# Optimization experiments

Measured on AMD Instinct MI355X. Metric: run time of the kernel, lower is better.

The kernel has to match this reference:

```python
import jax, jax.numpy as jnp
import numpy as np

B, T, NE, NZ, H = 64, 1024, 256, 64, 256  # batch, timesteps, n_e, n_z, encoder_hidden
SW_HID = 128  # switch MLP hidden width (hardcoded in source)


def setup_inputs() -> dict:
    key = jax.random.key(0)
    ks = jax.random.split(key, 16)
    s = 0.05
    p = lambda k, shape: (jax.random.normal(k, shape, dtype=jnp.float32) * s)
    return {
        "e_seq": jax.random.normal(ks[0], (B, T, NE), dtype=jnp.float32),
        "eps": jax.random.normal(ks[1], (B, T, NZ), dtype=jnp.float32),  # randn_like noise, precomputed
        # GRU forward direction (torch layout: weight_ih [3H, NE] order r,z,n)
        "w_ih_f": p(ks[2], (3 * H, NE)), "w_hh_f": p(ks[3], (3 * H, H)),
        "b_ih_f": jnp.zeros((3 * H,), jnp.float32), "b_hh_f": jnp.zeros((3 * H,), jnp.float32),
        # GRU backward direction
        "w_ih_b": p(ks[4], (3 * H, NE)), "w_hh_b": p(ks[5], (3 * H, H)),
        "b_ih_b": jnp.zeros((3 * H,), jnp.float32), "b_hh_b": jnp.zeros((3 * H,), jnp.float32),
        # mu / logvar heads over [B,T,2H]
        "mu_w": p(ks[6], (NZ, 2 * H)), "mu_b": jnp.zeros((NZ,), jnp.float32),
        "lv_w": p(ks[7], (NZ, 2 * H)), "lv_b": jnp.zeros((NZ,), jnp.float32),
        # switching unit: Linear(NE + 2H + NZ, 128) -> ReLU -> Linear(128,1) -> Sigmoid
        "sw_w1": p(ks[8], (SW_HID, NE + 2 * H + NZ)), "sw_b1": jnp.zeros((SW_HID,), jnp.float32),
        "sw_w2": p(ks[9], (1, SW_HID)), "sw_b2": jnp.zeros((1,), jnp.float32),
    }


def _gru_dir(x, w_ih, w_hh, b_ih, b_hh, reverse):
    # x: [B,T,NE]; torch GRU cell: r,z = sigmoid; n = tanh(x_n + r*(W_hn h + b_hn)); h' = (1-z)*n + z*h
    xp = jnp.einsum('btn,gn->btg', x, w_ih) + b_ih  # [B,T,3H] input projections, once
    xp = jnp.swapaxes(xp, 0, 1)  # [T,B,3H]
    h0 = jnp.zeros((x.shape[0], w_hh.shape[1]), x.dtype)

    def step(h, xpt):
        hp = h @ w_hh.T + b_hh
        xr, xz, xn = jnp.split(xpt, 3, axis=-1)
        hr, hz, hn = jnp.split(hp, 3, axis=-1)
        r = jax.nn.sigmoid(xr + hr)
        z = jax.nn.sigmoid(xz + hz)
        n = jnp.tanh(xn + r * hn)
        h_new = (1.0 - z) * n + z * h
        return h_new, h_new

    _, hs = jax.lax.scan(step, h0, xp, reverse=reverse)  # outputs time-aligned even when reversed
    return jnp.swapaxes(hs, 0, 1)  # [B,T,H]


def _forward(e_seq, eps, w_ih_f, w_hh_f, b_ih_f, b_hh_f, w_ih_b, w_hh_b, b_ih_b, b_hh_b,
             mu_w, mu_b, lv_w, lv_b, sw_w1, sw_b1, sw_w2, sw_b2):
    h_f = _gru_dir(e_seq, w_ih_f, w_hh_f, b_ih_f, b_hh_f, reverse=False)
    h_b = _gru_dir(e_seq, w_ih_b, w_hh_b, b_ih_b, b_hh_b, reverse=True)
    h_seq = jnp.concatenate([h_f, h_b], axis=-1)  # [B,T,2H]

    mu = h_seq @ mu_w.T + mu_b    # [B,T,NZ]
    lv = h_seq @ lv_w.T + lv_b    # [B,T,NZ]

    n_e = e_seq.shape[-1]
    h2 = h_seq.shape[-1]
    # split switch first-layer weight by input segments [e_t | h_t | z_prev]
    w1_e = sw_w1[:, :n_e]
    w1_h = sw_w1[:, n_e:n_e + h2]
    w1_z = sw_w1[:, n_e + h2:]
    # precompute e/h contributions for all t; only z_prev contribution is sequential
    pre = jnp.einsum('btn,kn->btk', e_seq, w1_e) + jnp.einsum('bth,kh->btk', h_seq, w1_h) + sw_b1  # [B,T,128]

    z_tilde = mu + jnp.exp(0.5 * lv) * eps                    # reparameterized sample [B,T,NZ]
    kl = (-0.5 * (1.0 + lv - mu * mu - jnp.exp(lv))).sum(-1)  # [B,T]

    def step(z_prev, inputs):
        pre_t, zt_t = inputs  # [B,128], [B,NZ]
        hid = jax.nn.relu(pre_t + z_prev @ w1_z.T)
        beta = jax.nn.sigmoid(hid @ sw_w2.T + sw_b2)[..., 0]  # [B]
        z_t = beta[:, None] * zt_t + (1.0 - beta[:, None]) * z_prev
        return z_t, (z_t, beta)

    z0 = jnp.zeros((e_seq.shape[0], mu.shape[-1]), e_seq.dtype)
    _, (zs, betas) = jax.lax.scan(step, z0, (jnp.swapaxes(pre, 0, 1), jnp.swapaxes(z_tilde, 0, 1)))
    z_seq = jnp.swapaxes(zs, 0, 1)     # [B,T,NZ]
    beta_seq = jnp.swapaxes(betas, 0, 1)  # [B,T]
    kl_loss = kl.mean()
    return z_seq, kl_loss, beta_seq


def reference(e_seq, eps, w_ih_f, w_hh_f, b_ih_f, b_hh_f, w_ih_b, w_hh_b, b_ih_b, b_hh_b,
              mu_w, mu_b, lv_w, lv_b, sw_w1, sw_b1, sw_w2, sw_b2):
    return _forward(e_seq, eps, w_ih_f, w_hh_f, b_ih_f, b_hh_f, w_ih_b, w_hh_b, b_ih_b, b_hh_b,
                    mu_w, mu_b, lv_w, lv_b, sw_w1, sw_b1, sw_w2, sw_b2)
```

## Files before the change

### kernel.cpp

```cpp
#include <hip/hip_runtime.h>
#include <cstdint>

typedef _Float16 half_t;
typedef _Float16 half2_t __attribute__((ext_vector_type(2)));
typedef _Float16 h8_t __attribute__((ext_vector_type(8)));
typedef float f4_t __attribute__((ext_vector_type(4)));
typedef unsigned int uint32;
typedef uint32 uv16 __attribute__((ext_vector_type(16)));

static constexpr int B_ = 64, T_ = 1024;

#define DEV __device__ __forceinline__

DEV float fdot2f(half2_t a, half2_t b, float c) {
#if __has_builtin(__builtin_amdgcn_fdot2)
  return __builtin_amdgcn_fdot2(a, b, c, false);
#else
  return fmaf((float)a.x, (float)b.x, fmaf((float)a.y, (float)b.y, c));
#endif
}

DEV float fast_rcp(float x) { return __builtin_amdgcn_rcpf(x); }
DEV float sigmf(float x) { return fast_rcp(1.f + __expf(-x)); }
DEV float tanhf_(float x) { return 1.f - 2.f * fast_rcp(1.f + __expf(2.f * x)); }
DEV uint32 pack2(float a, float b) {
  half2_t h; h.x = (half_t)a; h.y = (half_t)b;
  return __builtin_bit_cast(uint32, h);
}
DEV half2_t bch2(uint32 u) { return __builtin_bit_cast(half2_t, u); }

DEV void gload_lds16(const void* g, void* l) {
  __builtin_amdgcn_global_load_lds(
      (const __attribute__((address_space(1))) uint32*)g,
      (__attribute__((address_space(3))) uint32*)l, 16, 0, 0);
}

#define WSEL(va, vb, j) bch2(((j) < 16) ? (va)[(j) & 15] : (vb)[((j) - 16) & 15])

__global__ __launch_bounds__(256) void pack_w(
    const float* __restrict__ w_ih_f, const float* __restrict__ w_ih_b,
    const float* __restrict__ mu_w, const float* __restrict__ lv_w,
    const float* __restrict__ sw_w1,
    const float* __restrict__ w_hh_f, const float* __restrict__ w_hh_b,
    const float* __restrict__ b_ih_f, const float* __restrict__ b_ih_b,
    const float* __restrict__ b_hh_f, const float* __restrict__ b_hh_b,
    const float* __restrict__ mu_b, const float* __restrict__ lv_b,
    const float* __restrict__ sw_b1,
    uint32* __restrict__ wihf, uint32* __restrict__ wihb,
    uint32* __restrict__ wchf, uint32* __restrict__ wchb, uint32* __restrict__ wce2,
    uint32* __restrict__ whh, uint32* __restrict__ w1z,
    float* __restrict__ biasc, float* __restrict__ biasf, float* __restrict__ biasb) {
  int id = blockIdx.x * 256 + threadIdx.x;
  if (id < 98304) { wihf[id] = pack2(w_ih_f[2*id], w_ih_f[2*id+1]); return; }
  id -= 98304;
  if (id < 98304) { wihb[id] = pack2(w_ih_b[2*id], w_ih_b[2*id+1]); return; }
  id -= 98304;
  if (id < 32768) {
    int n = id >> 7, c0 = (id & 127) * 2;
    const float* p = (n < 64)  ? mu_w + n * 512 + c0
                   : (n < 128) ? lv_w + (n - 64) * 512 + c0
                               : sw_w1 + (n - 128) * 832 + 256 + c0;
    wchf[id] = pack2(p[0], p[1]); return;
  }
  id -= 32768;
  if (id < 32768) {
    int n = id >> 7, c0 = (id & 127) * 2;
    const float* p = (n < 64)  ? mu_w + n * 512 + 256 + c0
                   : (n < 128) ? lv_w + (n - 64) * 512 + 256 + c0
                               : sw_w1 + (n - 128) * 832 + 512 + c0;
    wchb[id] = pack2(p[0], p[1]); return;
  }
  id -= 32768;
  if (id < 16384) {
    int n = id >> 7, c0 = (id & 127) * 2;
    wce2[id] = pack2(sw_w1[n * 832 + c0], sw_w1[n * 832 + c0 + 1]); return;
  }
  id -= 16384;
  if (id < 196608) {
    int dd = id / 98304, q = id % 98304;
    int j = q >> 9, t2 = q & 511;
    int rr = t2 >> 2, pp = t2 & 3;
    int gi = j >> 5, ck = j & 31;
    int g = gi >> 1, i = gi & 1;
    int row = 256 * g + 2 * rr + i;
    int k0 = pp * 64 + 2 * ck;
    const float* w = dd ? w_hh_b : w_hh_f;
    whh[id] = pack2(w[row * 256 + k0], w[row * 256 + k0 + 1]);
    return;
  }
  id -= 196608;
  if (id < 4096) {
    int j = id >> 6, kk = id & 63;
    int row = (j < 32) ? kk : kk + 64;
    int jj = j & 31;
    w1z[id] = pack2(sw_w1[row * 832 + 768 + 2 * jj], sw_w1[row * 832 + 768 + 2 * jj + 1]);
    return;
  }
  id -= 4096;
  if (id < 256) {
    biasc[id] = (id < 64) ? mu_b[id] : (id < 128) ? lv_b[id - 64] : sw_b1[id - 128];
    return;
  }
  id -= 256;
  if (id < 768) { biasf[id] = b_ih_f[id] + (id < 512 ? b_hh_f[id] : 0.f); return; }
  id -= 768;
  if (id < 768) { biasb[id] = b_ih_b[id] + (id < 512 ? b_hh_b[id] : 0.f); return; }
}

template <int AF32, int ACC>
__global__ __launch_bounds__(256) void gemm_t(
    const void* __restrict__ Ap, int lda,
    const half_t* __restrict__ Bw,
    const float* __restrict__ bias,
    half_t* __restrict__ C, int ldc, int K) {
  __shared__ __align__(16) half_t smem[16384];
  half_t* As = smem;
  half_t* Bs = smem + 8192;
  const int tid = threadIdx.x;
  const int lane = tid & 63, w = tid >> 6;
  const int n0 = blockIdx.x * 128, m0 = blockIdx.y * 128;
  const int r8 = lane >> 3, c8 = lane & 7;
  f4_t acc[4][4];
  f4_t zero = {0.f, 0.f, 0.f, 0.f};
#pragma unroll
  for (int i = 0; i < 4; ++i)
#pragma unroll
    for (int j = 0; j < 4; ++j) acc[i][j] = zero;
  const int wm = (w >> 1) * 64, wn = (w & 1) * 64;
  for (int ks = 0; ks < K; ks += 64) {
    if constexpr (AF32) {
      const float* Af = (const float*)Ap;
#pragma unroll
      for (int it = 0; it < 4; ++it) {
        int c = it * 256 + tid;
        int row = c >> 3, coff = (c & 7) * 8;
        const float* ap = Af + (size_t)(m0 + row) * lda + ks + coff;
        float4 v0 = *(const float4*)ap;
        float4 v1 = *(const float4*)(ap + 4);
        uint4 u;
        u.x = pack2(v0.x, v0.y); u.y = pack2(v0.z, v0.w);
        u.z = pack2(v1.x, v1.y); u.w = pack2(v1.z, v1.w);
        *(uint4*)&As[(size_t)c * 8] = u;
      }
    } else {
      const half_t* Af = (const half_t*)Ap;
#pragma unroll
      for (int c = 0; c < 4; ++c) {
        int row = w * 32 + c * 8 + r8;
        gload_lds16(Af + (size_t)(m0 + row) * lda + ks + c8 * 8, As + (w * 4 + c) * 512);
      }
    }
#pragma unroll
    for (int c = 0; c < 4; ++c) {
      int row = w * 32 + c * 8 + r8;
      gload_lds16(Bw + (size_t)(n0 + row) * K + ks + c8 * 8, Bs + (w * 4 + c) * 512);
    }
    __syncthreads();
#pragma unroll
    for (int kk = 0; kk < 2; ++kk) {
      h8_t af[4], bf[4];
      const int ko = kk * 32 + (lane >> 4) * 8;
#pragma unroll
      for (int i = 0; i < 4; ++i) af[i] = *(const h8_t*)&As[(wm + i * 16 + (lane & 15)) * 64 + ko];
#pragma unroll
      for (int j = 0; j < 4; ++j) bf[j] = *(const h8_t*)&Bs[(wn + j * 16 + (lane & 15)) * 64 + ko];
#pragma unroll
      for (int i = 0; i < 4; ++i)
#pragma unroll
        for (int j = 0; j < 4; ++j)
          acc[i][j] = __builtin_amdgcn_mfma_f32_16x16x32_f16(af[i], bf[j], acc[i][j], 0, 0, 0);
    }
    __syncthreads();
  }
  const int cl4 = lane & 15, rl4 = lane >> 4;
#pragma unroll
  for (int j = 0; j < 4; ++j) {
    float bj = bias ? bias[n0 + wn + j * 16 + cl4] : 0.f;
#pragma unroll
    for (int i = 0; i < 4; ++i)
#pragma unroll
      for (int q = 0; q < 4; ++q) {
        int rl = wm + i * 16 + rl4 * 4 + q;
        int cc = wn + j * 16 + cl4;
        smem[rl * 128 + cc] = (half_t)(acc[i][j][q] + bj);
      }
  }
  __syncthreads();
#pragma unroll
  for (int it = 0; it < 8; ++it) {
    int idx = it * 256 + tid;
    int row = idx >> 4, colc = idx & 15;
    uint4 v = *(const uint4*)&smem[row * 128 + colc * 8];
    half_t* cp = C + (size_t)(m0 + row) * ldc + n0 + colc * 8;
    if constexpr (ACC) {
      uint4 o = *(const uint4*)cp;
      h8_t vv = __builtin_bit_cast(h8_t, v) + __builtin_bit_cast(h8_t, o);
      v = __builtin_bit_cast(uint4, vv);
    }
    *(uint4*)cp = v;
  }
}

__global__ __attribute__((amdgpu_flat_work_group_size(512, 512)))
__attribute__((amdgpu_waves_per_eu(2, 2))) void gru_rec(
    uint32* __restrict__ xp,
    const uint32* __restrict__ whh2,
    const float* __restrict__ bhh_f, const float* __restrict__ bhh_b) {
  const int wg = blockIdx.x;
  const int d = wg >> 6, b = wg & 63;
  const int tid = threadIdx.x;
  const int r = tid >> 2, p = tid & 3;
  __shared__ uint32 hb[2][144];
  if (tid < 144) { hb[0][tid] = 0; hb[1][tid] = 0; }
  uv16 w0a, w0b, w1a, w1b, w2a, w2b, w3a, w3b, w4a, w4b, w5a, w5b;
  {
    const uint32* wp = whh2 + (size_t)d * 98304 + tid;
#define LD16(vec, base)                                   \
  _Pragma("unroll") for (int e = 0; e < 16; ++e) vec[e] = \
      wp[(size_t)((base) + e) * 512];
    LD16(w0a, 0);   LD16(w0b, 16);  LD16(w1a, 32);  LD16(w1b, 48);
    LD16(w2a, 64);  LD16(w2b, 80);  LD16(w3a, 96);  LD16(w3b, 112);
    LD16(w4a, 128); LD16(w4b, 144); LD16(w5a, 160); LD16(w5b, 176);
#undef LD16
    asm volatile("" : "+v"(w0a), "+v"(w0b), "+v"(w1a), "+v"(w1b), "+v"(w2a), "+v"(w2b));
    asm volatile("" : "+v"(w3a), "+v"(w3b), "+v"(w4a), "+v"(w4b), "+v"(w5a), "+v"(w5b));
  }
  const float* bhh = d ? bhh_b : bhh_f;
  const float bhn0 = bhh[512 + 2 * r], bhn1 = bhh[512 + 2 * r + 1];
  uint32* xpu = xp + ((size_t)d * B_ + b) * T_ * 384;
  float h0 = 0.f, h1 = 0.f;
  const int dt = d ? -1 : 1;
  int t = d ? (T_ - 1) : 0;
  uint32 xr_n = 0, xz_n = 0, xn_n = 0;
  if (p == 0) {
    const uint32* rowp = xpu + (size_t)t * 384;
    xr_n = rowp[r]; xz_n = rowp[128 + r]; xn_n = rowp[256 + r];
  }
  const int rdbase = p * 36;
  const int wslice = (r >> 5) * 36 + (r & 31);
  __syncthreads();
  for (int step = 0; step < T_; ++step) {
    const int cur = step & 1;
    const uint32 xr = xr_n, xz = xz_n, xn = xn_n;
    const int tn = (step < T_ - 1) ? (t + dt) : t;
    if (p == 0) {
      const uint32* rowp = xpu + (size_t)tn * 384;
      xr_n = rowp[r]; xz_n = rowp[128 + r]; xn_n = rowp[256 + r];
    }
    float a00 = 0, a10 = 0, a01 = 0, a11 = 0, a02 = 0, a12 = 0;
    const uint32* hc = &hb[cur][rdbase];
#pragma unroll
    for (int c = 0; c < 4; ++c) {
      uint4 u0 = *(const uint4*)(hc + c * 8);
      uint4 u1 = *(const uint4*)(hc + c * 8 + 4);
      uint32 hv[8] = {u0.x, u0.y, u0.z, u0.w, u1.x, u1.y, u1.z, u1.w};
#pragma unroll
      for (int e = 0; e < 8; ++e) {
        const int j = c * 8 + e;
        half2_t hh = bch2(hv[e]);
        a00 = fdot2f(WSEL(w0a, w0b, j), hh, a00);
        a10 = fdot2f(WSEL(w1a, w1b, j), hh, a10);
        a01 = fdot2f(WSEL(w2a, w2b, j), hh, a01);
        a11 = fdot2f(WSEL(w3a, w3b, j), hh, a11);
        a02 = fdot2f(WSEL(w4a, w4b, j), hh, a02);
        a12 = fdot2f(WSEL(w5a, w5b, j), hh, a12);
      }
    }
    a00 += __shfl_xor(a00, 1); a00 += __shfl_xor(a00, 2);
    a10 += __shfl_xor(a10, 1); a10 += __shfl_xor(a10, 2);
    a01 += __shfl_xor(a01, 1); a01 += __shfl_xor(a01, 2);
    a11 += __shfl_xor(a11, 1); a11 += __shfl_xor(a11, 2);
    a02 += __shfl_xor(a02, 1); a02 += __shfl_xor(a02, 2);
    a12 += __shfl_xor(a12, 1); a12 += __shfl_xor(a12, 2);
    if (p == 0) {
      half2_t xrv = bch2(xr), xzv = bch2(xz), xnv = bch2(xn);
      float r0 = sigmf((float)xrv.x + a00);
      float z0 = sigmf((float)xzv.x + a01);
      float n0 = tanhf_((float)xnv.x + r0 * (a02 + bhn0));
      h0 = (1.f - z0) * n0 + z0 * h0;
      float r1 = sigmf((float)xrv.y + a10);
      float z1 = sigmf((float)xzv.y + a11);
      float n1 = tanhf_((float)xnv.y + r1 * (a12 + bhn1));
      h1 = (1.f - z1) * n1 + z1 * h1;
      uint32 ph = pack2(h0, h1);
      hb[cur ^ 1][wslice] = ph;
      xpu[(size_t)t * 384 + r] = ph;
    }
    __syncthreads();
    t = tn;
  }
}

__global__ __launch_bounds__(256) void zkl(const half_t* __restrict__ hp,
                                           const float* __restrict__ eps,
                                           float* __restrict__ ztil,
                                           float* __restrict__ klp) {
  const int blk = blockIdx.x, tid = threadIdx.x;
  const size_t bt = (size_t)blk * 4 + (tid >> 6);
  const int j = tid & 63;
  float mu = (float)hp[bt * 768 + j];
  float lv = (float)hp[bt * 768 + 64 + j];
  float ev = eps[bt * 64 + j];
  ztil[bt * 64 + j] = mu + __expf(0.5f * lv) * ev;
  float term = 1.f + lv - mu * mu - __expf(lv);
#pragma unroll
  for (int s = 1; s < 64; s <<= 1) term += __shfl_xor(term, s);
  __shared__ float red[4];
  if ((tid & 63) == 0) red[tid >> 6] = term;
  __syncthreads();
  if (tid == 0) klp[blk] = red[0] + red[1] + red[2] + red[3];
}

__global__ __launch_bounds__(256) void klred(const float* __restrict__ klp,
                                             float* __restrict__ out) {
  const int tid = threadIdx.x;
  float s = 0.f;
  for (int i = tid; i < 16384; i += 256) s += klp[i];
#pragma unroll
  for (int st = 1; st < 64; st <<= 1) s += __shfl_xor(s, st);
  __shared__ float red[4];
  if ((tid & 63) == 0) red[tid >> 6] = s;
  __syncthreads();
  if (tid == 0) out[0] = (red[0] + red[1] + red[2] + red[3]) * (-0.5f / 65536.f);
}

__global__ __launch_bounds__(64) void z_scan(
    const half_t* __restrict__ hp,
    const float* __restrict__ zt_arr,
    const uint32* __restrict__ w1z,
    const float* __restrict__ sw_w2, const float* __restrict__ sw_b2,
    float* __restrict__ z_out, float* __restrict__ beta_out) {
  const int b = blockIdx.x;
  const int k = threadIdx.x;
  uv16 z0a, z0b, z1a, z1b;
  {
#define LDZ(vec, base)                                    \
  _Pragma("unroll") for (int e = 0; e < 16; ++e) vec[e] = \
      w1z[((base) + e) * 64 + k];
    LDZ(z0a, 0); LDZ(z0b, 16); LDZ(z1a, 32); LDZ(z1b, 48);
#undef LDZ
    asm volatile("" : "+v"(z0a), "+v"(z0b), "+v"(z1a), "+v"(z1b));
  }
  const float w2k0 = sw_w2[k], w2k1 = sw_w2[k + 64], b2 = sw_b2[0];
  __shared__ uint32 zbuf[2][32];
  if (k < 32) { zbuf[0][k] = 0; zbuf[1][k] = 0; }
  __syncthreads();
  float zf = 0.f;
  const size_t bt0 = (size_t)b * T_;
  float pre0n = (float)hp[bt0 * 768 + 128 + k];
  float pre1n = (float)hp[bt0 * 768 + 192 + k];
  float ztn = zt_arr[bt0 * 64 + k];
  for (int t = 0; t < T_; ++t) {
    const int cur = t & 1;
    const float pre0 = pre0n, pre1 = pre1n, zt = ztn;
    const int tn = (t < T_ - 1) ? t + 1 : t;
    pre0n = (float)hp[(bt0 + tn) * 768 + 128 + k];
    pre1n = (float)hp[(bt0 + tn) * 768 + 192 + k];
    ztn = zt_arr[(bt0 + tn) * 64 + k];
    float a0 = 0, a1 = 0, a2 = 0, a3 = 0;
#pragma unroll
    for (int q = 0; q < 8; ++q) {
      uint4 u = *(const uint4*)&zbuf[cur][q * 4];
      const int m = q * 4;
      a0 = fdot2f(WSEL(z0a, z0b, m),     bch2(u.x), a0);
      a1 = fdot2f(WSEL(z0a, z0b, m + 1), bch2(u.y), a1);
      a0 = fdot2f(WSEL(z0a, z0b, m + 2), bch2(u.z), a0);
      a1 = fdot2f(WSEL(z0a, z0b, m + 3), bch2(u.w), a1);
      a2 = fdot2f(WSEL(z1a, z1b, m),     bch2(u.x), a2);
      a3 = fdot2f(WSEL(z1a, z1b, m + 1), bch2(u.y), a3);
      a2 = fdot2f(WSEL(z1a, z1b, m + 2), bch2(u.z), a2);
      a3 = fdot2f(WSEL(z1a, z1b, m + 3), bch2(u.w), a3);
    }
    float hid0 = fmaxf(pre0 + a0 + a1, 0.f);
    float hid1 = fmaxf(pre1 + a2 + a3, 0.f);
    float v = fmaf(hid0, w2k0, hid1 * w2k1);
#pragma unroll
    for (int s = 1; s < 64; s <<= 1) v += __shfl_xor(v, s);
    const float beta = sigmf(v + b2);
    zf = beta * zt + (1.f - beta) * zf;
    z_out[(bt0 + t) * 64 + k] = zf;
    if (k == 0) beta_out[bt0 + t] = beta;
    float zo = __shfl_xor(zf, 1);
    if ((k & 1) == 0) zbuf[cur ^ 1][k >> 1] = pack2(zf, zo);
    asm volatile("s_waitcnt lgkmcnt(0)" ::: "memory");
  }
}

extern "C" void kernel_launch(void* const* d_in, const int* in_sizes, int n_in,
                              void* d_out, int out_size, void* d_ws, size_t ws_size,
                              hipStream_t stream) {
  (void)in_sizes; (void)n_in; (void)out_size;
  const float* e_seq  = (const float*)d_in[0];
  const float* eps    = (const float*)d_in[1];
  const float* w_ih_f = (const float*)d_in[2];
  const float* w_hh_f = (const float*)d_in[3];
  const float* b_ih_f = (const float*)d_in[4];
  const float* b_hh_f = (const float*)d_in[5];
  const float* w_ih_b = (const float*)d_in[6];
  const float* w_hh_b = (const float*)d_in[7];
  const float* b_ih_b = (const float*)d_in[8];
  const float* b_hh_b = (const float*)d_in[9];
  const float* mu_w   = (const float*)d_in[10];
  const float* mu_b   = (const float*)d_in[11];
  const float* lv_w   = (const float*)d_in[12];
  const float* lv_b   = (const float*)d_in[13];
  const float* sw_w1  = (const float*)d_in[14];
  const float* sw_b1  = (const float*)d_in[15];
  const float* sw_w2  = (const float*)d_in[16];
  const float* sw_b2  = (const float*)d_in[17];

  const size_t NEED = 201326592 + 1924096;
  if (ws_size < NEED) return;
  char* ws = (char*)d_ws;
  half_t* xpf = (half_t*)ws;
  half_t* xpb = (half_t*)(ws + 100663296);
  half_t* hp  = xpf + 512;
  float*  ztil = (float*)(ws + 100663296);
  float*  klp  = (float*)(ws + 100663296 + 16777216);
  char* wr = ws + 201326592;
  uint32* wihf  = (uint32*)(wr);
  uint32* wihb  = (uint32*)(wr + 393216);
  uint32* wchf  = (uint32*)(wr + 786432);
  uint32* wchb  = (uint32*)(wr + 917504);
  uint32* wce2  = (uint32*)(wr + 1048576);
  uint32* whh2  = (uint32*)(wr + 1114112);
  uint32* w1z2  = (uint32*)(wr + 1900544);
  float*  biasc = (float*)(wr + 1916928);
  float*  biasf = (float*)(wr + 1917952);
  float*  biasb = (float*)(wr + 1921024);

  pack_w<<<1879, 256, 0, stream>>>(w_ih_f, w_ih_b, mu_w, lv_w, sw_w1, w_hh_f, w_hh_b,
                                   b_ih_f, b_ih_b, b_hh_f, b_hh_b, mu_b, lv_b, sw_b1,
                                   wihf, wihb, wchf, wchb, wce2, whh2, w1z2,
                                   biasc, biasf, biasb);
  gemm_t<1, 0><<<dim3(6, 512), 256, 0, stream>>>(e_seq, 256, (const half_t*)wihf, biasf, xpf, 768, 256);
  gemm_t<1, 0><<<dim3(6, 512), 256, 0, stream>>>(e_seq, 256, (const half_t*)wihb, biasb, xpb, 768, 256);
  gru_rec<<<128, 512, 0, stream>>>((uint32*)ws, whh2, b_hh_f, b_hh_b);
  gemm_t<0, 0><<<dim3(2, 512), 256, 0, stream>>>(xpf, 768, (const half_t*)wchf, biasc, hp, 768, 256);
  gemm_t<0, 1><<<dim3(2, 512), 256, 0, stream>>>(xpb, 768, (const half_t*)wchb, nullptr, hp, 768, 256);
  gemm_t<1, 1><<<dim3(1, 512), 256, 0, stream>>>(e_seq, 256, (const half_t*)wce2, nullptr, hp + 128, 768, 256);
  zkl<<<16384, 256, 0, stream>>>(hp, eps, ztil, klp);
  klred<<<1, 256, 0, stream>>>(klp, (float*)d_out + 4194304);
  z_scan<<<64, 64, 0, stream>>>(hp, ztil, w1z2, sw_w2, sw_b2, (float*)d_out, (float*)d_out + 4194305);
}
```

Measured before the change: 2.103 ms.

## Keep GRU recurrent weights in AGPRs and relax occupancy hints

Moves the 192 per-thread recurrent weight words of gru_rec out of VGPRs into accumulation registers with inline-asm accvgpr writes, and reads each back just before its fdot2. waves_per_eu is relaxed to (1,2) so the compiler has more room for the larger register set. z_scan drops its register-pinning asm barrier and gets a min-blocks launch bound. The intent is to free VGPR pressure and avoid spills or awkward vector selects. In exchange, every dot product now needs an extra v_accvgpr_read, and the volatile asm may limit instruction scheduling on the latency-critical serial recurrence.

```diff
diff --git a/kernel.cpp b/kernel.cpp
--- a/kernel.cpp
+++ b/kernel.cpp
@@ -201,8 +201,34 @@
   }
 }
 
+#define W_ALL(X) \
+  X(0) X(1) X(2) X(3) X(4) X(5) X(6) X(7) X(8) X(9) X(10) X(11) X(12) X(13) X(14) X(15) \
+  X(16) X(17) X(18) X(19) X(20) X(21) X(22) X(23) X(24) X(25) X(26) X(27) X(28) X(29) X(30) X(31) \
+  X(32) X(33) X(34) X(35) X(36) X(37) X(38) X(39) X(40) X(41) X(42) X(43) X(44) X(45) X(46) X(47) \
+  X(48) X(49) X(50) X(51) X(52) X(53) X(54) X(55) X(56) X(57) X(58) X(59) X(60) X(61) X(62) X(63) \
+  X(64) X(65) X(66) X(67) X(68) X(69) X(70) X(71) X(72) X(73) X(74) X(75) X(76) X(77) X(78) X(79) \
+  X(80) X(81) X(82) X(83) X(84) X(85) X(86) X(87) X(88) X(89) X(90) X(91) X(92) X(93) X(94) X(95) \
+  X(96) X(97) X(98) X(99) X(100) X(101) X(102) X(103) X(104) X(105) X(106) X(107) X(108) X(109) X(110) X(111) \
+  X(112) X(113) X(114) X(115) X(116) X(117) X(118) X(119) X(120) X(121) X(122) X(123) X(124) X(125) X(126) X(127) \
+  X(128) X(129) X(130) X(131) X(132) X(133) X(134) X(135) X(136) X(137) X(138) X(139) X(140) X(141) X(142) X(143) \
+  X(144) X(145) X(146) X(147) X(148) X(149) X(150) X(151) X(152) X(153) X(154) X(155) X(156) X(157) X(158) X(159) \
+  X(160) X(161) X(162) X(163) X(164) X(165) X(166) X(167) X(168) X(169) X(170) X(171) X(172) X(173) X(174) X(175) \
+  X(176) X(177) X(178) X(179) X(180) X(181) X(182) X(183) X(184) X(185) X(186) X(187) X(188) X(189) X(190) X(191)
+
+#define WDECL(n) uint32 wa##n;
+#define WLOAD(n) asm volatile("v_accvgpr_write_b32 %0, %1" : "=a"(wa##n) : "v"(wp[(n) * 512]));
+#define DOT(W, hh, acc)                                                  \
+  do {                                                                   \
+    uint32 _t;                                                           \
+    asm volatile("v_accvgpr_read_b32 %0, %1" : "=v"(_t) : "a"(W));       \
+    acc = fdot2f(bch2(_t), (hh), (acc));                                 \
+  } while (0)
+#define SIX(j0, j1, j2, j3, j4, j5, hh)  \
+  DOT(wa##j0, hh, a00); DOT(wa##j1, hh, a10); DOT(wa##j2, hh, a01); \
+  DOT(wa##j3, hh, a11); DOT(wa##j4, hh, a02); DOT(wa##j5, hh, a12);
+
 __global__ __attribute__((amdgpu_flat_work_group_size(512, 512)))
-__attribute__((amdgpu_waves_per_eu(2, 2))) void gru_rec(
+__attribute__((amdgpu_waves_per_eu(1, 2))) void gru_rec(
     uint32* __restrict__ xp,
     const uint32* __restrict__ whh2,
     const float* __restrict__ bhh_f, const float* __restrict__ bhh_b) {
@@ -212,18 +238,10 @@
   const int r = tid >> 2, p = tid & 3;
   __shared__ uint32 hb[2][144];
   if (tid < 144) { hb[0][tid] = 0; hb[1][tid] = 0; }
-  uv16 w0a, w0b, w1a, w1b, w2a, w2b, w3a, w3b, w4a, w4b, w5a, w5b;
+  W_ALL(WDECL)
   {
     const uint32* wp = whh2 + (size_t)d * 98304 + tid;
-#define LD16(vec, base)                                   \
-  _Pragma("unroll") for (int e = 0; e < 16; ++e) vec[e] = \
-      wp[(size_t)((base) + e) * 512];
-    LD16(w0a, 0);   LD16(w0b, 16);  LD16(w1a, 32);  LD16(w1b, 48);
-    LD16(w2a, 64);  LD16(w2b, 80);  LD16(w3a, 96);  LD16(w3b, 112);
-    LD16(w4a, 128); LD16(w4b, 144); LD16(w5a, 160); LD16(w5b, 176);
-#undef LD16
-    asm volatile("" : "+v"(w0a), "+v"(w0b), "+v"(w1a), "+v"(w1b), "+v"(w2a), "+v"(w2b));
-    asm volatile("" : "+v"(w3a), "+v"(w3b), "+v"(w4a), "+v"(w4b), "+v"(w5a), "+v"(w5b));
+    W_ALL(WLOAD)
   }
   const float* bhh = d ? bhh_b : bhh_f;
   const float bhn0 = bhh[512 + 2 * r], bhn1 = bhh[512 + 2 * r + 1];
@@ -249,22 +267,61 @@
     }
     float a00 = 0, a10 = 0, a01 = 0, a11 = 0, a02 = 0, a12 = 0;
     const uint32* hc = &hb[cur][rdbase];
-#pragma unroll
-    for (int c = 0; c < 4; ++c) {
-      uint4 u0 = *(const uint4*)(hc + c * 8);
-      uint4 u1 = *(const uint4*)(hc + c * 8 + 4);
-      uint32 hv[8] = {u0.x, u0.y, u0.z, u0.w, u1.x, u1.y, u1.z, u1.w};
-#pragma unroll
-      for (int e = 0; e < 8; ++e) {
-        const int j = c * 8 + e;
-        half2_t hh = bch2(hv[e]);
-        a00 = fdot2f(WSEL(w0a, w0b, j), hh, a00);
-        a10 = fdot2f(WSEL(w1a, w1b, j), hh, a10);
-        a01 = fdot2f(WSEL(w2a, w2b, j), hh, a01);
-        a11 = fdot2f(WSEL(w3a, w3b, j), hh, a11);
-        a02 = fdot2f(WSEL(w4a, w4b, j), hh, a02);
-        a12 = fdot2f(WSEL(w5a, w5b, j), hh, a12);
-      }
+    {
+      uint4 u0 = *(const uint4*)(hc + 0);
+      uint4 u1 = *(const uint4*)(hc + 4);
+      half2_t g0 = bch2(u0.x), g1 = bch2(u0.y), g2 = bch2(u0.z), g3 = bch2(u0.w);
+      half2_t g4 = bch2(u1.x), g5 = bch2(u1.y), g6 = bch2(u1.z), g7 = bch2(u1.w);
+      SIX(0, 32, 64, 96, 128, 160, g0)
+      SIX(1, 33, 65, 97, 129, 161, g1)
+      SIX(2, 34, 66, 98, 130, 162, g2)
+      SIX(3, 35, 67, 99, 131, 163, g3)
+      SIX(4, 36, 68, 100, 132, 164, g4)
+      SIX(5, 37, 69, 101, 133, 165, g5)
+      SIX(6, 38, 70, 102, 134, 166, g6)
+      SIX(7, 39, 71, 103, 135, 167, g7)
+    }
+    {
+      uint4 u0 = *(const uint4*)(hc + 8);
+      uint4 u1 = *(const uint4*)(hc + 12);
+      half2_t g0 = bch2(u0.x), g1 = bch2(u0.y), g2 = bch2(u0.z), g3 = bch2(u0.w);
+      half2_t g4 = bch2(u1.x), g5 = bch2(u1.y), g6 = bch2(u1.z), g7 = bch2(u1.w);
+      SIX(8, 40, 72, 104, 136, 168, g0)
+      SIX(9, 41, 73, 105, 137, 169, g1)
+      SIX(10, 42, 74, 106, 138, 170, g2)
+      SIX(11, 43, 75, 107, 139, 171, g3)
+      SIX(12, 44, 76, 108, 140, 172, g4)
+      SIX(13, 45, 77, 109, 141, 173, g5)
+      SIX(14, 46, 78, 110, 142, 174, g6)
+      SIX(15, 47, 79, 111, 143, 175, g7)
+    }
+    {
+      uint4 u0 = *(const uint4*)(hc + 16);
+      uint4 u1 = *(const uint4*)(hc + 20);
+      half2_t g0 = bch2(u0.x), g1 = bch2(u0.y), g2 = bch2(u0.z), g3 = bch2(u0.w);
+      half2_t g4 = bch2(u1.x), g5 = bch2(u1.y), g6 = bch2(u1.z), g7 = bch2(u1.w);
+      SIX(16, 48, 80, 112, 144, 176, g0)
+      SIX(17, 49, 81, 113, 145, 177, g1)
+      SIX(18, 50, 82, 114, 146, 178, g2)
+      SIX(19, 51, 83, 115, 147, 179, g3)
+      SIX(20, 52, 84, 116, 148, 180, g4)
+      SIX(21, 53, 85, 117, 149, 181, g5)
+      SIX(22, 54, 86, 118, 150, 182, g6)
+      SIX(23, 55, 87, 119, 151, 183, g7)
+    }
+    {
+      uint4 u0 = *(const uint4*)(hc + 24);
+      uint4 u1 = *(const uint4*)(hc + 28);
+      half2_t g0 = bch2(u0.x), g1 = bch2(u0.y), g2 = bch2(u0.z), g3 = bch2(u0.w);
+      half2_t g4 = bch2(u1.x), g5 = bch2(u1.y), g6 = bch2(u1.z), g7 = bch2(u1.w);
+      SIX(24, 56, 88, 120, 152, 184, g0)
+      SIX(25, 57, 89, 121, 153, 185, g1)
+      SIX(26, 58, 90, 122, 154, 186, g2)
+      SIX(27, 59, 91, 123, 155, 187, g3)
+      SIX(28, 60, 92, 124, 156, 188, g4)
+      SIX(29, 61, 93, 125, 157, 189, g5)
+      SIX(30, 62, 94, 126, 158, 190, g6)
+      SIX(31, 63, 95, 127, 159, 191, g7)
     }
     a00 += __shfl_xor(a00, 1); a00 += __shfl_xor(a00, 2);
     a10 += __shfl_xor(a10, 1); a10 += __shfl_xor(a10, 2);
@@ -324,7 +381,7 @@
   if (tid == 0) out[0] = (red[0] + red[1] + red[2] + red[3]) * (-0.5f / 65536.f);
 }
 
-__global__ __launch_bounds__(64) void z_scan(
+__global__ __launch_bounds__(64, 4) void z_scan(
     const half_t* __restrict__ hp,
     const float* __restrict__ zt_arr,
     const uint32* __restrict__ w1z,
@@ -339,7 +396,6 @@
       w1z[((base) + e) * 64 + k];
     LDZ(z0a, 0); LDZ(z0b, 16); LDZ(z1a, 32); LDZ(z1b, 48);
 #undef LDZ
-    asm volatile("" : "+v"(z0a), "+v"(z0b), "+v"(z1a), "+v"(z1b));
   }
   const float w2k0 = sw_w2[k], w2k1 = sw_w2[k + 64], b2 = sw_b2[0];
   __shared__ uint32 zbuf[2][32];
```

Result: slower. 3.261 ms (+55.1%).
